# Kernel tuning notes

Hardware: AMD Instinct MI355X
Metric: run time of the kernel (lower is better)

Reference implementation:

```python
import jax, jax.numpy as jnp
import numpy as np

B = 32768  # batch of sudoku puzzles

def _pair_matrices():
    # 36 = C(9,2) digit-pair permutations, exactly as in the torch __init__
    enc = np.zeros((36, 9), dtype=np.float32)
    dec = np.zeros((9, 36), dtype=np.float32)
    count = 0
    for i in range(8):
        for j in range(i + 1, 9):
            enc[count, i] = 1.0
            enc[count, j] = 1.0
            dec[i, count] = 1.0
            dec[j, count] = 1.0
            count += 1
    return enc, dec

def nn_and(x, y):
    return jnp.clip(jnp.minimum(x, y), 0.0, 1.0)

def nn_compare(x, value):
    # triangular bump: 1 at x==value, 0 outside (value-1, value+1)
    a = jax.nn.relu(x - value + 1.0)
    b = jax.nn.relu(value + 1.0 - x)
    return jnp.minimum(a, b)

def setup_inputs() -> dict:
    key = jax.random.key(0)
    # binary candidate mask: mask[b, d, r, c] == 1 iff digit d is still possible at (r, c)
    mask = jnp.round(jax.random.uniform(key, (B, 9, 9, 9), dtype=jnp.float32))
    enc, dec = _pair_matrices()
    return {"mask": mask, "enc_w": jnp.asarray(enc), "dec_w": jnp.asarray(dec)}

def reference(mask, enc_w, dec_w):
    # encode_permutations: 1x1 conv 9 -> 36 channels
    perm = jnp.einsum("oc,bchw->bohw", enc_w, mask)          # [B,36,9,9]
    perm = nn_compare(perm, 2.0)                              # cell has exactly this digit-pair
    # sum_all_permutations: 1x1 conv 36 -> 1 with all-ones weight
    s = jnp.sum(perm, axis=1, keepdims=True)                  # [B,1,9,9]
    s = nn_compare(s, 1.0)
    perm = nn_and(perm, s)                                    # broadcast over 36 channels
    # type 'h': grouped (1,9) all-ones conv = sum over width
    down = jnp.sum(perm, axis=3, keepdims=True)               # [B,36,9,1]
    down = nn_compare(down, 2.0)
    # UpsamplingNearest2d(scale_factor=(1,9)) of a width-1 map = broadcast
    up = jnp.broadcast_to(down, perm.shape)                   # [B,36,9,9]
    up = nn_and(up, 1.0 - perm)                               # NNNot(perm)
    # decode_permutations: 1x1 conv 36 -> 9
    erase = jnp.einsum("oc,bchw->bohw", dec_w, up)            # [B,9,9,9]
    return nn_and(mask, 1.0 - erase)
```

## Files before the change

### kernel.cpp

```cpp
#include <hip/hip_runtime.h>
#include <stdint.h>


#define WAVE_BATCHES 4
#define WAVE_WORDS (WAVE_BATCHES * 729)
#define WAVE_CHUNKS (WAVE_WORDS / 4)
#define WAVES_PER_WG 4

typedef uint32_t u32x4 __attribute__((ext_vector_type(4)));
typedef const __attribute__((address_space(1))) uint32_t* gsrc_t;
typedef __attribute__((address_space(3))) uint32_t* lptr_t;

__global__ __launch_bounds__(256) void sudoku_kernel(
    const uint32_t* __restrict__ in, uint32_t* __restrict__ out, int nwaves) {
  __shared__ __align__(16) uint32_t lds[WAVES_PER_WG][WAVE_WORDS];
  const int lane = threadIdx.x & 63;
  const int wslot = threadIdx.x >> 6;
  const int wave_id = blockIdx.x * WAVES_PER_WG + wslot;
  if (wave_id >= nwaves) return;

  const uint32_t* gin = in + (size_t)wave_id * WAVE_WORDS;
  uint32_t* lbase = &lds[wslot][0];

#pragma unroll
  for (int j = 0; j < 12; ++j) {
    int i = lane + j * 64;
    if (i < WAVE_CHUNKS) {
      __builtin_amdgcn_global_load_lds((gsrc_t)(gin + i * 4),
                                       (lptr_t)(lbase + i * 4), 16, 0, 0);
    }
  }
  asm volatile("s_waitcnt vmcnt(0)" ::: "memory");

  if (lane < WAVE_BATCHES * 9) {
    const int bl = lane / 9;
    const int h = lane - bl * 9;
    const int rbase = bl * 729 + h * 9;

    uint32_t cand[9];
#pragma unroll
    for (int w = 0; w < 9; ++w) cand[w] = 0u;
#pragma unroll
    for (int d = 0; d < 9; ++d) {
#pragma unroll
      for (int w = 0; w < 9; ++w)
        cand[w] |= (lbase[rbase + d * 81 + w] ? 1u : 0u) << d;
    }

    uint32_t clearbits[9];
#pragma unroll
    for (int w = 0; w < 9; ++w) clearbits[w] = 0u;
#pragma unroll
    for (int w1 = 0; w1 < 9; ++w1) {
      uint32_t c1 = cand[w1];
      if (__popc(c1) != 2) continue;
      int cnt = 0;
#pragma unroll
      for (int w2 = 0; w2 < 9; ++w2) cnt += (cand[w2] == c1) ? 1 : 0;
      if (cnt == 2) {
#pragma unroll
        for (int w = 0; w < 9; ++w)
          if (cand[w] != c1) clearbits[w] |= c1;
      }
    }

    uint32_t keep[9];
#pragma unroll
    for (int w = 0; w < 9; ++w) keep[w] = cand[w] & ~clearbits[w];

#pragma unroll
    for (int d = 0; d < 9; ++d) {
#pragma unroll
      for (int w = 0; w < 9; ++w)
        lbase[rbase + d * 81 + w] = ((keep[w] >> d) & 1u) ? 0x3F800000u : 0u;
    }
  }

  uint32_t* gout = out + (size_t)wave_id * WAVE_WORDS;
#pragma unroll
  for (int j = 0; j < 12; ++j) {
    int i = lane + j * 64;
    if (i < WAVE_CHUNKS) {
      u32x4 v = *(const u32x4*)(lbase + i * 4);
      *(u32x4*)(gout + i * 4) = v;
    }
  }
}

extern "C" void kernel_launch(void* const* d_in, const int* in_sizes, int n_in,
                              void* d_out, int out_size, void* d_ws, size_t ws_size,
                              hipStream_t stream) {
  const uint32_t* in = (const uint32_t*)d_in[0];
  uint32_t* out = (uint32_t*)d_out;
  int B = in_sizes[0] / 729;
  int nwaves = (B + WAVE_BATCHES - 1) / WAVE_BATCHES;
  int blocks = (nwaves + WAVES_PER_WG - 1) / WAVES_PER_WG;
  sudoku_kernel<<<blocks, 256, 0, stream>>>(in, out, nwaves);
}
```

Baseline: 35.56 us.

## Double-buffer LDS per wave to overlap DMA loads with compute and stores

Each wave now processes four units of four puzzles in sequence. Two LDS buffers let the global-to-LDS DMA for the next unit stay in flight while the current unit is computed and written back, with hand-placed vmcnt and lgkmcnt waits to order the phases. Workgroups shrink to two waves, so the grid has far fewer waves and relies on in-wave overlap rather than occupancy to hide memory latency. Tail bounds checks are removed, so the batch size must divide evenly into the new units.

```diff
diff --git a/kernel.cpp b/kernel.cpp
--- a/kernel.cpp
+++ b/kernel.cpp
@@ -2,37 +2,30 @@
 #include <stdint.h>
 
 
-#define WAVE_BATCHES 4
-#define WAVE_WORDS (WAVE_BATCHES * 729)
-#define WAVE_CHUNKS (WAVE_WORDS / 4)
-#define WAVES_PER_WG 4
+#define UNIT_BATCHES 4
+#define UNIT_WORDS (UNIT_BATCHES * 729)
+#define UNIT_CHUNKS (UNIT_WORDS / 4)
+#define UNITS_PER_WAVE 4
+#define WAVES_PER_WG 2
 
 typedef uint32_t u32x4 __attribute__((ext_vector_type(4)));
 typedef const __attribute__((address_space(1))) uint32_t* gsrc_t;
 typedef __attribute__((address_space(3))) uint32_t* lptr_t;
 
-__global__ __launch_bounds__(256) void sudoku_kernel(
-    const uint32_t* __restrict__ in, uint32_t* __restrict__ out, int nwaves) {
-  __shared__ __align__(16) uint32_t lds[WAVES_PER_WG][WAVE_WORDS];
-  const int lane = threadIdx.x & 63;
-  const int wslot = threadIdx.x >> 6;
-  const int wave_id = blockIdx.x * WAVES_PER_WG + wslot;
-  if (wave_id >= nwaves) return;
-
-  const uint32_t* gin = in + (size_t)wave_id * WAVE_WORDS;
-  uint32_t* lbase = &lds[wslot][0];
-
+__device__ __forceinline__ void issue_dma(const uint32_t* gin, uint32_t* lbase,
+                                          int lane) {
 #pragma unroll
   for (int j = 0; j < 12; ++j) {
     int i = lane + j * 64;
-    if (i < WAVE_CHUNKS) {
+    if (i < UNIT_CHUNKS) {
       __builtin_amdgcn_global_load_lds((gsrc_t)(gin + i * 4),
                                        (lptr_t)(lbase + i * 4), 16, 0, 0);
     }
   }
-  asm volatile("s_waitcnt vmcnt(0)" ::: "memory");
+}
 
-  if (lane < WAVE_BATCHES * 9) {
+__device__ __forceinline__ void compute_unit(uint32_t* lbase, int lane) {
+  if (lane < UNIT_BATCHES * 9) {
     const int bl = lane / 9;
     const int h = lane - bl * 9;
     const int rbase = bl * 729 + h * 9;
@@ -64,25 +57,57 @@
       }
     }
 
-    uint32_t keep[9];
-#pragma unroll
-    for (int w = 0; w < 9; ++w) keep[w] = cand[w] & ~clearbits[w];
-
 #pragma unroll
     for (int d = 0; d < 9; ++d) {
 #pragma unroll
-      for (int w = 0; w < 9; ++w)
-        lbase[rbase + d * 81 + w] = ((keep[w] >> d) & 1u) ? 0x3F800000u : 0u;
+      for (int w = 0; w < 9; ++w) {
+        uint32_t k = (cand[w] & ~clearbits[w]) >> d;
+        lbase[rbase + d * 81 + w] = (k & 1u) ? 0x3F800000u : 0u;
+      }
     }
   }
+}
 
-  uint32_t* gout = out + (size_t)wave_id * WAVE_WORDS;
+__device__ __forceinline__ void store_unit(const uint32_t* lbase,
+                                           uint32_t* gout, int lane) {
 #pragma unroll
   for (int j = 0; j < 12; ++j) {
     int i = lane + j * 64;
-    if (i < WAVE_CHUNKS) {
+    if (i < UNIT_CHUNKS) {
       u32x4 v = *(const u32x4*)(lbase + i * 4);
       *(u32x4*)(gout + i * 4) = v;
+    }
+  }
+}
+
+__global__ __launch_bounds__(WAVES_PER_WG * 64) void sudoku_kernel(
+    const uint32_t* __restrict__ in, uint32_t* __restrict__ out) {
+  __shared__ __align__(16) uint32_t lds[WAVES_PER_WG][2][UNIT_WORDS];
+  const int lane = threadIdx.x & 63;
+  const int wslot = threadIdx.x >> 6;
+  const int wave_id = blockIdx.x * WAVES_PER_WG + wslot;
+  const size_t base_unit = (size_t)wave_id * UNITS_PER_WAVE;
+
+  uint32_t* buf0 = &lds[wslot][0][0];
+  uint32_t* buf1 = &lds[wslot][1][0];
+
+  issue_dma(in + (base_unit + 0) * UNIT_WORDS, buf0, lane);
+  issue_dma(in + (base_unit + 1) * UNIT_WORDS, buf1, lane);
+
+#pragma unroll
+  for (int u = 0; u < UNITS_PER_WAVE; ++u) {
+    uint32_t* cur = (u & 1) ? buf1 : buf0;
+    if (u == 0 || u == UNITS_PER_WAVE - 1)
+      asm volatile("s_waitcnt vmcnt(12)" ::: "memory");
+    else
+      asm volatile("s_waitcnt vmcnt(24)" ::: "memory");
+
+    compute_unit(cur, lane);
+    store_unit(cur, out + (base_unit + u) * UNIT_WORDS, lane);
+
+    if (u + 2 < UNITS_PER_WAVE) {
+      asm volatile("s_waitcnt lgkmcnt(0)" ::: "memory");
+      issue_dma(in + (base_unit + u + 2) * UNIT_WORDS, cur, lane);
     }
   }
 }
@@ -93,7 +118,8 @@
   const uint32_t* in = (const uint32_t*)d_in[0];
   uint32_t* out = (uint32_t*)d_out;
   int B = in_sizes[0] / 729;
-  int nwaves = (B + WAVE_BATCHES - 1) / WAVE_BATCHES;
-  int blocks = (nwaves + WAVES_PER_WG - 1) / WAVES_PER_WG;
-  sudoku_kernel<<<blocks, 256, 0, stream>>>(in, out, nwaves);
+  int nunits = B / UNIT_BATCHES;
+  int nwaves = nunits / UNITS_PER_WAVE;
+  int blocks = nwaves / WAVES_PER_WG;
+  sudoku_kernel<<<blocks, WAVES_PER_WG * 64, 0, stream>>>(in, out);
 }
```

After: 43.21 us. 21.5% more time.
